# Optimization experiments

Hardware: AMD Instinct MI355X
Metric: run time of the kernel (lower is better)

Reference implementation:

```python
import jax, jax.numpy as jnp
import numpy as np

N_NODES = 100000
N_EDGES = 3200000
N_FEAT = 256
HIDDEN = 64
N_CLASSES = 6


def gcn_conv(x, W, b, src, dst, n_nodes):
    """PyG GCNConv: out = D^{-1/2} (A + I) D^{-1/2} X W + b (self-loops added)."""
    h = x @ W  # [N, out]
    loops = jnp.arange(n_nodes, dtype=src.dtype)
    src2 = jnp.concatenate([src, loops])
    dst2 = jnp.concatenate([dst, loops])
    # degree over destination nodes (edge weight 1), including self-loops
    deg = jax.ops.segment_sum(jnp.ones_like(dst2, dtype=h.dtype), dst2,
                              num_segments=n_nodes)
    dis = jnp.where(deg > 0, jax.lax.rsqrt(deg), 0.0)  # deg^{-1/2}
    norm = dis[src2] * dis[dst2]  # [E+N]
    msg = h[src2] * norm[:, None]  # gather + scale
    out = jax.ops.segment_sum(msg, dst2, num_segments=n_nodes)  # scatter-add
    return out + b


def setup_inputs() -> dict:
    key = jax.random.key(0)
    ks = jax.random.split(key, 5)
    x = jax.random.normal(ks[0], (N_NODES, N_FEAT), dtype=jnp.float32)
    edge_index = jax.random.randint(ks[1], (2, N_EDGES), 0, N_NODES, dtype=jnp.int64)
    W1 = jax.random.normal(ks[2], (N_FEAT, HIDDEN), dtype=jnp.float32) / np.sqrt(N_FEAT)
    b1 = jnp.zeros((HIDDEN,), dtype=jnp.float32)
    W2 = jax.random.normal(ks[3], (HIDDEN, HIDDEN), dtype=jnp.float32) / np.sqrt(HIDDEN)
    b2 = jnp.zeros((HIDDEN,), dtype=jnp.float32)
    Wfc = jax.random.normal(ks[4], (HIDDEN, N_CLASSES), dtype=jnp.float32) / np.sqrt(HIDDEN)
    bfc = jnp.zeros((N_CLASSES,), dtype=jnp.float32)
    return {"x": x, "edge_index": edge_index, "W1": W1, "b1": b1,
            "W2": W2, "b2": b2, "Wfc": Wfc, "bfc": bfc}


def reference(x, edge_index, W1, b1, W2, b2, Wfc, bfc):
    src, dst = edge_index[0], edge_index[1]
    n = x.shape[0]
    h = jax.nn.relu(gcn_conv(x, W1, b1, src, dst, n))
    # dropout(p=0.2) is identity in eval mode
    h = jax.nn.relu(gcn_conv(h, W2, b2, src, dst, n))
    return h @ Wfc + bfc
```

## Files before the change

### kernel.cpp

```cpp
#include <hip/hip_runtime.h>
#include <hip/hip_fp16.h>
#include <math.h>

#define NFEAT 256
#define HID 64
#define NCLS 6
#define CAP 4096
#define NBMX 1600
#define RCAP 8
#define CHUNK 16384
#define BT 1024
#define ROUND (BT * 4)

typedef float vf4 __attribute__((ext_vector_type(4)));
typedef int   vi4 __attribute__((ext_vector_type(4)));


__global__ __launch_bounds__(256) void k_zero_int(int* __restrict__ p, int n) {
  int i = blockIdx.x * 256 + threadIdx.x;
  if (i < n) p[i] = 0;
}


__global__ __launch_bounds__(BT) void k_binpack(const int* __restrict__ src,
                                                const int* __restrict__ dst,
                                                int* __restrict__ gcur,
                                                unsigned* __restrict__ packed,
                                                int E, int nbuck) {
  __shared__ unsigned ring[NBMX * RCAP];
  __shared__ int basel[NBMX];
  int t = threadIdx.x;
  for (int i = t; i < nbuck; i += BT) basel[i] = 0;
  __syncthreads();

  int e0 = blockIdx.x * CHUNK;
  int e1 = e0 + CHUNK;
  if (e1 > E) e1 = E;

  for (int r0 = e0; r0 < e1; r0 += ROUND) {
    int i0 = r0 + t * 4;
    int s4[4], d4[4];
    bool full = (i0 + 4 <= e1);
    if (full) {
      vi4 sv = __builtin_nontemporal_load((const vi4*)&src[i0]);
      vi4 dv = __builtin_nontemporal_load((const vi4*)&dst[i0]);
      s4[0] = sv.x; s4[1] = sv.y; s4[2] = sv.z; s4[3] = sv.w;
      d4[0] = dv.x; d4[1] = dv.y; d4[2] = dv.z; d4[3] = dv.w;
    } else {
      for (int q = 0; q < 4; ++q)
        if (i0 + q < e1) { s4[q] = src[i0 + q]; d4[q] = dst[i0 + q]; }
    }
#pragma unroll
    for (int q = 0; q < 4; ++q) {
      if (i0 + q < e1) {
        int b = d4[q] >> 6;
        unsigned e = ((unsigned)s4[q] << 6) | (unsigned)(d4[q] & 63);
        int sl = atomicAdd(&basel[b], 1);
        if (sl < RCAP) ring[b * RCAP + sl] = e;
        else packed[(size_t)b * CAP + atomicAdd(&gcur[b], 1)] = e;
      }
    }
    __syncthreads();
    for (int b = t; b < nbuck; b += BT) {
      if (basel[b] >= RCAP) {
        int gb = atomicAdd(&gcur[b], RCAP);
        unsigned* pd = &packed[(size_t)b * CAP + gb];
#pragma unroll
        for (int k = 0; k < RCAP; ++k) pd[k] = ring[b * RCAP + k];
        basel[b] = 0;
      }
    }
    __syncthreads();
  }
  for (int b = t; b < nbuck; b += BT) {
    int m = basel[b];
    if (m > 0) {
      int gb = atomicAdd(&gcur[b], m);
      unsigned* pd = &packed[(size_t)b * CAP + gb];
      for (int k = 0; k < m; ++k) pd[k] = ring[b * RCAP + k];
    }
  }
}


__global__ __launch_bounds__(256) void k_scanb(const int* __restrict__ gcur,
                                               int* __restrict__ bbase, int nb,
                                               int* __restrict__ rowptr_n) {
  __shared__ int sh[256];
  __shared__ int carry;
  int t = threadIdx.x;
  if (t == 0) carry = 0;
  __syncthreads();
  for (int base = 0; base < nb; base += 256) {
    int v = 0;
    if (base + t < nb) {
      int c = gcur[base + t];
      v = (c > CAP) ? CAP : c;
    }
    sh[t] = v;
    __syncthreads();
    for (int off = 1; off < 256; off <<= 1) {
      int x = sh[t];
      int y = (t >= off) ? sh[t - off] : 0;
      __syncthreads();
      sh[t] = x + y;
      __syncthreads();
    }
    if (base + t < nb) bbase[base + t] = carry + sh[t] - v;
    __syncthreads();
    if (t == 255) carry += sh[255];
    __syncthreads();
  }
  if (t == 0) *rowptr_n = carry;
}


__global__ __launch_bounds__(256) void k_build(const unsigned* __restrict__ packed,
                                               const int* __restrict__ gcur,
                                               const int* __restrict__ bbase,
                                               int* __restrict__ rowptr,
                                               int* __restrict__ srcs,
                                               float* __restrict__ dis,
                                               int n, int nbuck) {
  __shared__ int cnt4[4][64];
  __shared__ int cur4[4][64];
  __shared__ int offx[64];
  __shared__ int offi[64];
  __shared__ int cntl[64];
  int b = blockIdx.x;
  int t = threadIdx.x;
  int g = t >> 6;
  int m = gcur[b];
  if (m > CAP) m = CAP;
#pragma unroll
  for (int i = 0; i < 1; ++i) cnt4[g][t & 63] = 0;
  __syncthreads();
  const unsigned* pb = packed + (size_t)b * CAP;

  for (int k = t; k < m; k += 256)
    atomicAdd(&cnt4[g][__builtin_nontemporal_load(&pb[k]) & 63u], 1);
  __syncthreads();
  if (t < 64) {
    int c0 = cnt4[0][t], c1 = cnt4[1][t], c2 = cnt4[2][t], c3 = cnt4[3][t];
    int tot = c0 + c1 + c2 + c3;
    cntl[t] = tot;
    offi[t] = tot;
    cur4[0][t] = 0;
    cur4[1][t] = c0;
    cur4[2][t] = c0 + c1;
    cur4[3][t] = c0 + c1 + c2;
  }
  __syncthreads();
  for (int off = 1; off < 64; off <<= 1) {
    int x = (t < 64) ? offi[t] : 0;
    int y = (t >= off && t < 64) ? offi[t - off] : 0;
    __syncthreads();
    if (t < 64) offi[t] = x + y;
    __syncthreads();
  }
  int bb = bbase[b];
  if (t < 64) {
    offx[t] = offi[t] - cntl[t];
    int v = b * 64 + t;
    if (v < n) {
      rowptr[v] = bb + offx[t];
      dis[v] = rsqrtf((float)cntl[t] + 1.0f);
    }
  }
  __syncthreads();
  if (t < 64) {
#pragma unroll
    for (int gg = 0; gg < 4; ++gg) cur4[gg][t] += offx[t];
  }
  __syncthreads();
  for (int k = t; k < m; k += 256) {
    unsigned e = pb[k];
    int dl = e & 63u;
    int q = atomicAdd(&cur4[g][dl], 1);
    srcs[bb + q] = (int)(e >> 6);
  }
}


template<int K>
__global__ __launch_bounds__(256) void k_gemm_scaled(const float* __restrict__ X,
                                                     const float* __restrict__ W,
                                                     const float* __restrict__ dis,
                                                     __half* __restrict__ G16, int n) {
  __shared__ float Wl[64 * 64];
  __shared__ float Xl[64 * 64];
  const int tid = threadIdx.x;
  const int row0 = blockIdx.x * 64;
  const int tc = tid & 15;
  const int tr = tid >> 4;
  float acc[4][4] = {};

  for (int k0 = 0; k0 < K; k0 += 64) {
    __syncthreads();
#pragma unroll
    for (int i = 0; i < 4; ++i) {
      int idx = tid * 4 + i * 1024;
      int kr = idx >> 6, c = idx & 63;
      *(float4*)&Wl[idx] = *(const float4*)&W[(size_t)(k0 + kr) * 64 + c];
    }
#pragma unroll
    for (int i = 0; i < 4; ++i) {
      int idx = tid * 4 + i * 1024;
      int r = idx >> 6, c = idx & 63;
      int row = row0 + r;
      vf4 v = {0.f, 0.f, 0.f, 0.f};
      if (row < n) v = __builtin_nontemporal_load((const vf4*)&X[(size_t)row * K + k0 + c]);
      *(vf4*)&Xl[idx] = v;
    }
    __syncthreads();
#pragma unroll 4
    for (int kk = 0; kk < 64; kk += 4) {
      float4 xv[4], wv[4];
#pragma unroll
      for (int r = 0; r < 4; ++r) xv[r] = *(float4*)&Xl[(tr * 4 + r) * 64 + kk];
#pragma unroll
      for (int q = 0; q < 4; ++q) wv[q] = *(float4*)&Wl[(kk + q) * 64 + tc * 4];
#pragma unroll
      for (int r = 0; r < 4; ++r) {
        const float xr[4] = {xv[r].x, xv[r].y, xv[r].z, xv[r].w};
#pragma unroll
        for (int q = 0; q < 4; ++q) {
          acc[r][0] += xr[q] * wv[q].x;
          acc[r][1] += xr[q] * wv[q].y;
          acc[r][2] += xr[q] * wv[q].z;
          acc[r][3] += xr[q] * wv[q].w;
        }
      }
    }
  }
#pragma unroll
  for (int r = 0; r < 4; ++r) {
    int row = row0 + tr * 4 + r;
    if (row < n) {
      float s = dis[row];
      __half2 h01 = __floats2half2_rn(acc[r][0] * s, acc[r][1] * s);
      __half2 h23 = __floats2half2_rn(acc[r][2] * s, acc[r][3] * s);
      uint2 st;
      st.x = *reinterpret_cast<unsigned*>(&h01);
      st.y = *reinterpret_cast<unsigned*>(&h23);
      ((uint2*)G16)[(size_t)row * 16 + tc] = st;
    }
  }
}


__global__ __launch_bounds__(256) void k_agg_csr(const int* __restrict__ rowptr,
                                                 const int* __restrict__ srcs,
                                                 const __half* __restrict__ g16,
                                                 const float* __restrict__ dis,
                                                 const float* __restrict__ bias,
                                                 float* __restrict__ outp, int n) {
  int v = blockIdx.x * 16 + (threadIdx.x >> 4);
  if (v >= n) return;
  int lane = threadIdx.x & 15;
  int beg = rowptr[v], end = rowptr[v + 1];
  const uint2* g2 = (const uint2*)g16;

  uint2 su = g2[(size_t)v * 16 + lane];
  float2 f0 = __half22float2(*reinterpret_cast<__half2*>(&su.x));
  float2 f1 = __half22float2(*reinterpret_cast<__half2*>(&su.y));
  float ax = f0.x, ay = f0.y, az = f1.x, aw = f1.y;

  int j = beg;
  for (; j + 8 <= end; j += 8) {
    int s[8];
#pragma unroll
    for (int q = 0; q < 8; ++q) s[q] = __builtin_nontemporal_load(&srcs[j + q]);
    uint2 a[8];
#pragma unroll
    for (int q = 0; q < 8; ++q) a[q] = g2[(size_t)s[q] * 16 + lane];
#pragma unroll
    for (int q = 0; q < 8; ++q) {
      float2 p0 = __half22float2(*reinterpret_cast<__half2*>(&a[q].x));
      float2 p1 = __half22float2(*reinterpret_cast<__half2*>(&a[q].y));
      ax += p0.x; ay += p0.y; az += p1.x; aw += p1.y;
    }
  }
  for (; j < end; ++j) {
    int s0 = __builtin_nontemporal_load(&srcs[j]);
    uint2 a0 = g2[(size_t)s0 * 16 + lane];
    float2 p0 = __half22float2(*reinterpret_cast<__half2*>(&a0.x));
    float2 p1 = __half22float2(*reinterpret_cast<__half2*>(&a0.y));
    ax += p0.x; ay += p0.y; az += p1.x; aw += p1.y;
  }

  float dv = dis[v];
  float4 bb = *(const float4*)&bias[lane * 4];
  float4 o;
  o.x = fmaxf(fmaf(dv, ax, bb.x), 0.f);
  o.y = fmaxf(fmaf(dv, ay, bb.y), 0.f);
  o.z = fmaxf(fmaf(dv, az, bb.z), 0.f);
  o.w = fmaxf(fmaf(dv, aw, bb.w), 0.f);
  ((float4*)outp)[(size_t)v * 16 + lane] = o;
}


__global__ __launch_bounds__(256) void k_fc(const float* __restrict__ A,
                                            const float* __restrict__ Wfc,
                                            const float* __restrict__ bfc,
                                            float* __restrict__ outp, int n) {
  __shared__ float Wl[64 * NCLS];
  __shared__ float bl[8];
  int tid = threadIdx.x;
  for (int i = tid; i < 64 * NCLS; i += 256) Wl[i] = Wfc[i];
  if (tid < NCLS) bl[tid] = bfc[tid];
  __syncthreads();
  int row = blockIdx.x * 256 + tid;
  if (row >= n) return;
  float accv[NCLS];
#pragma unroll
  for (int j = 0; j < NCLS; ++j) accv[j] = bl[j];
  const vf4* a4 = (const vf4*)&A[(size_t)row * 64];
#pragma unroll
  for (int k4 = 0; k4 < 16; ++k4) {
    vf4 a = __builtin_nontemporal_load(&a4[k4]);
    const float av[4] = {a.x, a.y, a.z, a.w};
#pragma unroll
    for (int q = 0; q < 4; ++q)
#pragma unroll
      for (int j = 0; j < NCLS; ++j) accv[j] += av[q] * Wl[(k4 * 4 + q) * NCLS + j];
  }
#pragma unroll
  for (int j = 0; j < NCLS; ++j) outp[(size_t)row * NCLS + j] = accv[j];
}


extern "C" void kernel_launch(void* const* d_in, const int* in_sizes, int n_in,
                              void* d_out, int out_size, void* d_ws, size_t ws_size,
                              hipStream_t stream) {
  const float* x   = (const float*)d_in[0];
  const int*   ei  = (const int*)d_in[1];
  const float* W1  = (const float*)d_in[2];
  const float* b1  = (const float*)d_in[3];
  const float* W2  = (const float*)d_in[4];
  const float* b2  = (const float*)d_in[5];
  const float* Wfc = (const float*)d_in[6];
  const float* bfc = (const float*)d_in[7];
  float* out = (float*)d_out;

  const int n = in_sizes[0] / NFEAT;
  const int E = in_sizes[1] / 2;
  const int* src = ei;
  const int* dst = ei + E;
  const int nbuck = (n + 63) >> 6;

  char* ws = (char*)d_ws;
  size_t off = 0;
  auto alloc = [&](size_t bytes) -> void* {
    void* p = (void*)(ws + off);
    off += (bytes + 255) & ~(size_t)255;
    return p;
  };
  float* dis    = (float*)alloc((size_t)n * 4);
  int*   rowptr = (int*)alloc(((size_t)n + 1) * 4);
  int*   srcs   = (int*)alloc((size_t)E * 4);
  int*   gcur   = (int*)alloc((size_t)nbuck * 4);
  int*   bbase  = (int*)alloc((size_t)nbuck * 4);
  size_t sharedBytes = (size_t)nbuck * CAP * 4;
  unsigned* packed = (unsigned*)alloc(sharedBytes);
  __half* bufA16 = (__half*)packed;
  float* bufB = (float*)alloc((size_t)n * HID * 4);

  k_zero_int<<<(nbuck + 255) / 256, 256, 0, stream>>>(gcur, nbuck);
  k_binpack<<<(E + CHUNK - 1) / CHUNK, BT, 0, stream>>>(src, dst, gcur, packed, E, nbuck);
  k_scanb<<<1, 256, 0, stream>>>(gcur, bbase, nbuck, rowptr + n);
  k_build<<<nbuck, 256, 0, stream>>>(packed, gcur, bbase, rowptr, srcs, dis, n, nbuck);

  k_gemm_scaled<NFEAT><<<(n + 63) / 64, 256, 0, stream>>>(x, W1, dis, bufA16, n);
  k_agg_csr<<<(n + 15) / 16, 256, 0, stream>>>(rowptr, srcs, bufA16, dis, b1, bufB, n);

  k_gemm_scaled<HID><<<(n + 63) / 64, 256, 0, stream>>>(bufB, W2, dis, bufA16, n);
  k_agg_csr<<<(n + 15) / 16, 256, 0, stream>>>(rowptr, srcs, bufA16, dis, b2, bufB, n);

  k_fc<<<(n + 255) / 256, 256, 0, stream>>>(bufB, Wfc, bfc, out, n);
}
```

Baseline: 354.2 us.

## Fuse edge binning with first GEMM and sort buckets in place

Merges the edge bin-packing pass and the first-layer X·W1 GEMM into one launch, with block ranges split by role, so the unscaled GEMM runs alongside edge binning. Because the GEMM no longer waits for degrees, the per-source normalisation moves into the first aggregation, which gathers dis[src] per edge. The global scan is dropped: each bucket is sorted in LDS and written back in place, and per-node (start, count) ranges replace rowptr. This removes a launch and a separate srcs array, at the cost of an extra dis gather per edge and lower binpack block size (256 threads, 1024-edge rounds).

```diff
diff --git a/kernel.cpp b/kernel.cpp
--- a/kernel.cpp
+++ b/kernel.cpp
@@ -9,8 +9,8 @@
 #define NBMX 1600
 #define RCAP 8
 #define CHUNK 16384
-#define BT 1024
-#define ROUND (BT * 4)
+#define ROUND 1024
+#define FUSED_LDS 57856
 
 typedef float vf4 __attribute__((ext_vector_type(4)));
 typedef int   vi4 __attribute__((ext_vector_type(4)));
@@ -22,123 +22,155 @@
 }
 
 
-__global__ __launch_bounds__(BT) void k_binpack(const int* __restrict__ src,
-                                                const int* __restrict__ dst,
-                                                int* __restrict__ gcur,
-                                                unsigned* __restrict__ packed,
-                                                int E, int nbuck) {
-  __shared__ unsigned ring[NBMX * RCAP];
-  __shared__ int basel[NBMX];
+__global__ __launch_bounds__(256) void k_fused(const int* __restrict__ src,
+                                               const int* __restrict__ dst,
+                                               int* __restrict__ gcur,
+                                               unsigned* __restrict__ packed,
+                                               int E, int nbuck, int nbb,
+                                               const float* __restrict__ X,
+                                               const float* __restrict__ W1,
+                                               __half* __restrict__ H16, int n) {
+  extern __shared__ char smem[];
   int t = threadIdx.x;
-  for (int i = t; i < nbuck; i += BT) basel[i] = 0;
-  __syncthreads();
-
-  int e0 = blockIdx.x * CHUNK;
-  int e1 = e0 + CHUNK;
-  if (e1 > E) e1 = E;
-
-  for (int r0 = e0; r0 < e1; r0 += ROUND) {
-    int i0 = r0 + t * 4;
-    int s4[4], d4[4];
-    bool full = (i0 + 4 <= e1);
-    if (full) {
-      vi4 sv = __builtin_nontemporal_load((const vi4*)&src[i0]);
-      vi4 dv = __builtin_nontemporal_load((const vi4*)&dst[i0]);
-      s4[0] = sv.x; s4[1] = sv.y; s4[2] = sv.z; s4[3] = sv.w;
-      d4[0] = dv.x; d4[1] = dv.y; d4[2] = dv.z; d4[3] = dv.w;
-    } else {
-      for (int q = 0; q < 4; ++q)
-        if (i0 + q < e1) { s4[q] = src[i0 + q]; d4[q] = dst[i0 + q]; }
-    }
-#pragma unroll
-    for (int q = 0; q < 4; ++q) {
-      if (i0 + q < e1) {
-        int b = d4[q] >> 6;
-        unsigned e = ((unsigned)s4[q] << 6) | (unsigned)(d4[q] & 63);
-        int sl = atomicAdd(&basel[b], 1);
-        if (sl < RCAP) ring[b * RCAP + sl] = e;
-        else packed[(size_t)b * CAP + atomicAdd(&gcur[b], 1)] = e;
-      }
-    }
+
+  if (blockIdx.x < nbb) {
+    unsigned* ring = (unsigned*)smem;
+    int* basel = (int*)(smem + NBMX * RCAP * 4);
+    for (int i = t; i < nbuck; i += 256) basel[i] = 0;
     __syncthreads();
-    for (int b = t; b < nbuck; b += BT) {
-      if (basel[b] >= RCAP) {
-        int gb = atomicAdd(&gcur[b], RCAP);
+
+    int e0 = blockIdx.x * CHUNK;
+    int e1 = e0 + CHUNK;
+    if (e1 > E) e1 = E;
+
+    for (int r0 = e0; r0 < e1; r0 += ROUND) {
+      int i0 = r0 + t * 4;
+      int s4[4], d4[4];
+      bool full = (i0 + 4 <= e1);
+      if (full) {
+        vi4 sv = __builtin_nontemporal_load((const vi4*)&src[i0]);
+        vi4 dv = __builtin_nontemporal_load((const vi4*)&dst[i0]);
+        s4[0] = sv.x; s4[1] = sv.y; s4[2] = sv.z; s4[3] = sv.w;
+        d4[0] = dv.x; d4[1] = dv.y; d4[2] = dv.z; d4[3] = dv.w;
+      } else {
+        for (int q = 0; q < 4; ++q)
+          if (i0 + q < e1) { s4[q] = src[i0 + q]; d4[q] = dst[i0 + q]; }
+      }
+#pragma unroll
+      for (int q = 0; q < 4; ++q) {
+        if (i0 + q < e1) {
+          int b = d4[q] >> 6;
+          unsigned e = ((unsigned)s4[q] << 6) | (unsigned)(d4[q] & 63);
+          int sl = atomicAdd(&basel[b], 1);
+          if (sl < RCAP) ring[b * RCAP + sl] = e;
+          else packed[(size_t)b * CAP + atomicAdd(&gcur[b], 1)] = e;
+        }
+      }
+      __syncthreads();
+      for (int b = t; b < nbuck; b += 256) {
+        if (basel[b] >= RCAP) {
+          int gb = atomicAdd(&gcur[b], RCAP);
+          unsigned* pd = &packed[(size_t)b * CAP + gb];
+#pragma unroll
+          for (int k = 0; k < RCAP; ++k) pd[k] = ring[b * RCAP + k];
+          basel[b] = 0;
+        }
+      }
+      __syncthreads();
+    }
+    for (int b = t; b < nbuck; b += 256) {
+      int m = basel[b];
+      if (m > 0) {
+        int gb = atomicAdd(&gcur[b], m);
         unsigned* pd = &packed[(size_t)b * CAP + gb];
-#pragma unroll
-        for (int k = 0; k < RCAP; ++k) pd[k] = ring[b * RCAP + k];
-        basel[b] = 0;
-      }
-    }
-    __syncthreads();
-  }
-  for (int b = t; b < nbuck; b += BT) {
-    int m = basel[b];
-    if (m > 0) {
-      int gb = atomicAdd(&gcur[b], m);
-      unsigned* pd = &packed[(size_t)b * CAP + gb];
-      for (int k = 0; k < m; ++k) pd[k] = ring[b * RCAP + k];
-    }
-  }
-}
-
-
-__global__ __launch_bounds__(256) void k_scanb(const int* __restrict__ gcur,
-                                               int* __restrict__ bbase, int nb,
-                                               int* __restrict__ rowptr_n) {
-  __shared__ int sh[256];
-  __shared__ int carry;
-  int t = threadIdx.x;
-  if (t == 0) carry = 0;
-  __syncthreads();
-  for (int base = 0; base < nb; base += 256) {
-    int v = 0;
-    if (base + t < nb) {
-      int c = gcur[base + t];
-      v = (c > CAP) ? CAP : c;
-    }
-    sh[t] = v;
-    __syncthreads();
-    for (int off = 1; off < 256; off <<= 1) {
-      int x = sh[t];
-      int y = (t >= off) ? sh[t - off] : 0;
+        for (int k = 0; k < m; ++k) pd[k] = ring[b * RCAP + k];
+      }
+    }
+  } else {
+    float* Wl = (float*)smem;
+    float* Xl = Wl + 4096;
+    const int row0 = (blockIdx.x - nbb) * 64;
+    const int tc = t & 15;
+    const int tr = t >> 4;
+    float acc[4][4] = {};
+
+    for (int k0 = 0; k0 < NFEAT; k0 += 64) {
       __syncthreads();
-      sh[t] = x + y;
+#pragma unroll
+      for (int i = 0; i < 4; ++i) {
+        int idx = t * 4 + i * 1024;
+        int kr = idx >> 6, c = idx & 63;
+        *(vf4*)&Wl[idx] = *(const vf4*)&W1[(size_t)(k0 + kr) * 64 + c];
+      }
+#pragma unroll
+      for (int i = 0; i < 4; ++i) {
+        int idx = t * 4 + i * 1024;
+        int r = idx >> 6, c = idx & 63;
+        int row = row0 + r;
+        vf4 v = {0.f, 0.f, 0.f, 0.f};
+        if (row < n) v = __builtin_nontemporal_load((const vf4*)&X[(size_t)row * NFEAT + k0 + c]);
+        *(vf4*)&Xl[idx] = v;
+      }
       __syncthreads();
-    }
-    if (base + t < nb) bbase[base + t] = carry + sh[t] - v;
-    __syncthreads();
-    if (t == 255) carry += sh[255];
-    __syncthreads();
-  }
-  if (t == 0) *rowptr_n = carry;
-}
-
-
-__global__ __launch_bounds__(256) void k_build(const unsigned* __restrict__ packed,
+#pragma unroll 4
+      for (int kk = 0; kk < 64; kk += 4) {
+        float4 xv[4], wv[4];
+#pragma unroll
+        for (int r = 0; r < 4; ++r) xv[r] = *(float4*)&Xl[(tr * 4 + r) * 64 + kk];
+#pragma unroll
+        for (int q = 0; q < 4; ++q) wv[q] = *(float4*)&Wl[(kk + q) * 64 + tc * 4];
+#pragma unroll
+        for (int r = 0; r < 4; ++r) {
+          const float xr[4] = {xv[r].x, xv[r].y, xv[r].z, xv[r].w};
+#pragma unroll
+          for (int q = 0; q < 4; ++q) {
+            acc[r][0] += xr[q] * wv[q].x;
+            acc[r][1] += xr[q] * wv[q].y;
+            acc[r][2] += xr[q] * wv[q].z;
+            acc[r][3] += xr[q] * wv[q].w;
+          }
+        }
+      }
+    }
+#pragma unroll
+    for (int r = 0; r < 4; ++r) {
+      int row = row0 + tr * 4 + r;
+      if (row < n) {
+        __half2 h01 = __floats2half2_rn(acc[r][0], acc[r][1]);
+        __half2 h23 = __floats2half2_rn(acc[r][2], acc[r][3]);
+        uint2 st;
+        st.x = *reinterpret_cast<unsigned*>(&h01);
+        st.y = *reinterpret_cast<unsigned*>(&h23);
+        ((uint2*)H16)[(size_t)row * 16 + tc] = st;
+      }
+    }
+  }
+}
+
+
+__global__ __launch_bounds__(256) void k_build(unsigned* __restrict__ packed,
                                                const int* __restrict__ gcur,
-                                               const int* __restrict__ bbase,
-                                               int* __restrict__ rowptr,
-                                               int* __restrict__ srcs,
+                                               int2* __restrict__ rowrange,
                                                float* __restrict__ dis,
                                                int n, int nbuck) {
+  __shared__ unsigned buf[CAP];
+  __shared__ unsigned outb[CAP];
   __shared__ int cnt4[4][64];
   __shared__ int cur4[4][64];
+  __shared__ int offi[64];
   __shared__ int offx[64];
-  __shared__ int offi[64];
   __shared__ int cntl[64];
   int b = blockIdx.x;
   int t = threadIdx.x;
   int g = t >> 6;
   int m = gcur[b];
   if (m > CAP) m = CAP;
-#pragma unroll
-  for (int i = 0; i < 1; ++i) cnt4[g][t & 63] = 0;
-  __syncthreads();
-  const unsigned* pb = packed + (size_t)b * CAP;
-
-  for (int k = t; k < m; k += 256)
-    atomicAdd(&cnt4[g][__builtin_nontemporal_load(&pb[k]) & 63u], 1);
+  unsigned* pb = packed + (size_t)b * CAP;
+
+  cnt4[g][t & 63] = 0;
+  for (int k = t; k < m; k += 256) buf[k] = pb[k];
+  __syncthreads();
+  for (int k = t; k < m; k += 256) atomicAdd(&cnt4[g][buf[k] & 63u], 1);
   __syncthreads();
   if (t < 64) {
     int c0 = cnt4[0][t], c1 = cnt4[1][t], c2 = cnt4[2][t], c3 = cnt4[3][t];
@@ -158,27 +190,80 @@
     if (t < 64) offi[t] = x + y;
     __syncthreads();
   }
-  int bb = bbase[b];
   if (t < 64) {
     offx[t] = offi[t] - cntl[t];
     int v = b * 64 + t;
     if (v < n) {
-      rowptr[v] = bb + offx[t];
+      rowrange[v] = make_int2(b * CAP + offx[t], cntl[t]);
       dis[v] = rsqrtf((float)cntl[t] + 1.0f);
     }
-  }
-  __syncthreads();
-  if (t < 64) {
 #pragma unroll
     for (int gg = 0; gg < 4; ++gg) cur4[gg][t] += offx[t];
   }
   __syncthreads();
   for (int k = t; k < m; k += 256) {
-    unsigned e = pb[k];
+    unsigned e = buf[k];
     int dl = e & 63u;
     int q = atomicAdd(&cur4[g][dl], 1);
-    srcs[bb + q] = (int)(e >> 6);
-  }
+    outb[q] = e >> 6;
+  }
+  __syncthreads();
+  for (int k = t; k < m; k += 256) pb[k] = outb[k];
+}
+
+
+__global__ __launch_bounds__(256) void k_agg_w(const int2* __restrict__ rowrange,
+                                               const int* __restrict__ srcs,
+                                               const __half* __restrict__ g16,
+                                               const float* __restrict__ dis,
+                                               const float* __restrict__ bias,
+                                               float* __restrict__ outp, int n) {
+  int v = blockIdx.x * 16 + (threadIdx.x >> 4);
+  if (v >= n) return;
+  int lane = threadIdx.x & 15;
+  int2 rr = rowrange[v];
+  int j = rr.x, end = rr.x + rr.y;
+  const uint2* g2 = (const uint2*)g16;
+
+  float dv = dis[v];
+  uint2 su = g2[(size_t)v * 16 + lane];
+  float2 f0 = __half22float2(*reinterpret_cast<__half2*>(&su.x));
+  float2 f1 = __half22float2(*reinterpret_cast<__half2*>(&su.y));
+  float ax = dv * f0.x, ay = dv * f0.y, az = dv * f1.x, aw = dv * f1.y;
+
+  for (; j + 8 <= end; j += 8) {
+    int s[8];
+#pragma unroll
+    for (int q = 0; q < 8; ++q) s[q] = __builtin_nontemporal_load(&srcs[j + q]);
+    float ds[8];
+    uint2 a[8];
+#pragma unroll
+    for (int q = 0; q < 8; ++q) { ds[q] = dis[s[q]]; a[q] = g2[(size_t)s[q] * 16 + lane]; }
+#pragma unroll
+    for (int q = 0; q < 8; ++q) {
+      float2 p0 = __half22float2(*reinterpret_cast<__half2*>(&a[q].x));
+      float2 p1 = __half22float2(*reinterpret_cast<__half2*>(&a[q].y));
+      ax = fmaf(ds[q], p0.x, ax); ay = fmaf(ds[q], p0.y, ay);
+      az = fmaf(ds[q], p1.x, az); aw = fmaf(ds[q], p1.y, aw);
+    }
+  }
+  for (; j < end; ++j) {
+    int s0 = __builtin_nontemporal_load(&srcs[j]);
+    float ds = dis[s0];
+    uint2 a0 = g2[(size_t)s0 * 16 + lane];
+    float2 p0 = __half22float2(*reinterpret_cast<__half2*>(&a0.x));
+    float2 p1 = __half22float2(*reinterpret_cast<__half2*>(&a0.y));
+    ax = fmaf(ds, p0.x, ax); ay = fmaf(ds, p0.y, ay);
+    az = fmaf(ds, p1.x, az); aw = fmaf(ds, p1.y, aw);
+  }
+
+  float4 bb = *(const float4*)&bias[lane * 4];
+  float4 o;
+  o.x = fmaxf(fmaf(dv, ax, bb.x), 0.f);
+  o.y = fmaxf(fmaf(dv, ay, bb.y), 0.f);
+  o.z = fmaxf(fmaf(dv, az, bb.z), 0.f);
+  o.w = fmaxf(fmaf(dv, aw, bb.w), 0.f);
+  ((float4*)outp)[(size_t)v * 16 + lane] = o;
 }
 
 
@@ -201,7 +286,7 @@
     for (int i = 0; i < 4; ++i) {
       int idx = tid * 4 + i * 1024;
       int kr = idx >> 6, c = idx & 63;
-      *(float4*)&Wl[idx] = *(const float4*)&W[(size_t)(k0 + kr) * 64 + c];
+      *(vf4*)&Wl[idx] = *(const vf4*)&W[(size_t)(k0 + kr) * 64 + c];
     }
 #pragma unroll
     for (int i = 0; i < 4; ++i) {
@@ -249,7 +334,7 @@
 }
 
 
-__global__ __launch_bounds__(256) void k_agg_csr(const int* __restrict__ rowptr,
+__global__ __launch_bounds__(256) void k_agg_csr(const int2* __restrict__ rowrange,
                                                  const int* __restrict__ srcs,
                                                  const __half* __restrict__ g16,
                                                  const float* __restrict__ dis,
@@ -258,7 +343,8 @@
   int v = blockIdx.x * 16 + (threadIdx.x >> 4);
   if (v >= n) return;
   int lane = threadIdx.x & 15;
-  int beg = rowptr[v], end = rowptr[v + 1];
+  int2 rr = rowrange[v];
+  int j = rr.x, end = rr.x + rr.y;
   const uint2* g2 = (const uint2*)g16;
 
   uint2 su = g2[(size_t)v * 16 + lane];
@@ -266,7 +352,6 @@
   float2 f1 = __half22float2(*reinterpret_cast<__half2*>(&su.y));
   float ax = f0.x, ay = f0.y, az = f1.x, aw = f1.y;
 
-  int j = beg;
   for (; j + 8 <= end; j += 8) {
     int s[8];
 #pragma unroll
@@ -348,6 +433,8 @@
   const int* src = ei;
   const int* dst = ei + E;
   const int nbuck = (n + 63) >> 6;
+  const int nbb = (E + CHUNK - 1) / CHUNK;
+  const int ntile = (n + 63) / 64;
 
   char* ws = (char*)d_ws;
   size_t off = 0;
@@ -356,26 +443,22 @@
     off += (bytes + 255) & ~(size_t)255;
     return p;
   };
-  float* dis    = (float*)alloc((size_t)n * 4);
-  int*   rowptr = (int*)alloc(((size_t)n + 1) * 4);
-  int*   srcs   = (int*)alloc((size_t)E * 4);
-  int*   gcur   = (int*)alloc((size_t)nbuck * 4);
-  int*   bbase  = (int*)alloc((size_t)nbuck * 4);
-  size_t sharedBytes = (size_t)nbuck * CAP * 4;
-  unsigned* packed = (unsigned*)alloc(sharedBytes);
-  __half* bufA16 = (__half*)packed;
-  float* bufB = (float*)alloc((size_t)n * HID * 4);
+  float* dis      = (float*)alloc((size_t)n * 4);
+  int2*  rowrange = (int2*)alloc((size_t)n * 8);
+  int*   gcur     = (int*)alloc((size_t)nbuck * 4);
+  unsigned* packed = (unsigned*)alloc((size_t)nbuck * CAP * 4);
+  __half* bufA16  = (__half*)alloc((size_t)n * HID * 2);
+  float* bufB     = (float*)alloc((size_t)n * HID * 4);
 
   k_zero_int<<<(nbuck + 255) / 256, 256, 0, stream>>>(gcur, nbuck);
-  k_binpack<<<(E + CHUNK - 1) / CHUNK, BT, 0, stream>>>(src, dst, gcur, packed, E, nbuck);
-  k_scanb<<<1, 256, 0, stream>>>(gcur, bbase, nbuck, rowptr + n);
-  k_build<<<nbuck, 256, 0, stream>>>(packed, gcur, bbase, rowptr, srcs, dis, n, nbuck);
-
-  k_gemm_scaled<NFEAT><<<(n + 63) / 64, 256, 0, stream>>>(x, W1, dis, bufA16, n);
-  k_agg_csr<<<(n + 15) / 16, 256, 0, stream>>>(rowptr, srcs, bufA16, dis, b1, bufB, n);
+  k_fused<<<nbb + ntile, 256, FUSED_LDS, stream>>>(src, dst, gcur, packed, E, nbuck, nbb,
+                                                   x, W1, bufA16, n);
+  k_build<<<nbuck, 256, 0, stream>>>(packed, gcur, rowrange, dis, n, nbuck);
+
+  k_agg_w<<<(n + 15) / 16, 256, 0, stream>>>(rowrange, (const int*)packed, bufA16, dis, b1, bufB, n);
 
   k_gemm_scaled<HID><<<(n + 63) / 64, 256, 0, stream>>>(bufB, W2, dis, bufA16, n);
-  k_agg_csr<<<(n + 15) / 16, 256, 0, stream>>>(rowptr, srcs, bufA16, dis, b2, bufB, n);
+  k_agg_csr<<<(n + 15) / 16, 256, 0, stream>>>(rowrange, (const int*)packed, bufA16, dis, b2, bufB, n);
 
   k_fc<<<(n + 255) / 256, 256, 0, stream>>>(bufB, Wfc, bfc, out, n);
 }
```

Result: faster. 319.8 us (-9.7%).
